# Kernel optimization log

Measured on AMD Instinct MI355X. Metric: run time of the kernel, lower is better.

The kernel has to match this reference:

```python
import jax, jax.numpy as jnp
import numpy as np

FACTOR = 5  # sampling factor from __init__


def setup_inputs() -> dict:
    key = jax.random.key(0)
    k1, k2, k3, k4 = jax.random.split(key, 4)
    B, L, H, D = 4, 2048, 8, 64
    S = min(FACTOR * int(np.ceil(np.log(L))), L)  # U_part = 40
    return {
        "queries": jax.random.normal(k1, (B, L, H, D), jnp.float32),
        "keys": jax.random.normal(k2, (B, L, H, D), jnp.float32),
        "values": jax.random.normal(k3, (B, L, H, D), jnp.float32),
        "index_sample": jax.random.randint(k4, (L, S), 0, L, jnp.int32),
    }


def reference(queries, keys, values, index_sample):
    B, L_Q, H, D = queries.shape
    L_K = keys.shape[1]
    Q = jnp.transpose(queries, (0, 2, 1, 3))  # [B,H,L_Q,D]
    K = jnp.transpose(keys, (0, 2, 1, 3))     # [B,H,L_K,D]
    V = jnp.transpose(values, (0, 2, 1, 3))   # [B,H,L_K,D]

    u = min(FACTOR * int(np.ceil(np.log(L_Q))), L_Q)  # n_top

    # --- _prob_QK: sampled QK to score queries, then top-u query selection ---
    # K_sample[b,h,q,s,:] = K[b,h,index_sample[q,s],:]  -> [B,H,L_Q,S,D]
    K_sample = K[:, :, index_sample, :]
    Q_K_sample = jnp.einsum('bhqd,bhqsd->bhqs', Q, K_sample)  # [B,H,L_Q,S]
    M = Q_K_sample.max(-1) - Q_K_sample.sum(-1) / L_K         # sparsity measure
    _, M_top = jax.lax.top_k(M, u)                            # [B,H,u] query indices

    Q_reduce = jnp.take_along_axis(Q, M_top[..., None], axis=2)  # [B,H,u,D]
    scale = 1.0 / np.sqrt(D)
    scores = jnp.einsum('bhud,bhkd->bhuk', Q_reduce, K) * scale  # [B,H,u,L_K]

    # --- _update_context causal mask: rows are the FIRST u rows of the full
    # triu(L_Q,L_Q) mask (faithful to original, which does NOT reindex by M_top)
    causal = jnp.triu(jnp.ones((u, L_Q), dtype=bool), 1)
    scores = jnp.where(causal[None, None], -jnp.inf, scores)
    attn = jax.nn.softmax(scores, axis=-1)
    upd = jnp.einsum('bhuk,bhkd->bhud', attn, V)  # [B,H,u,D]

    # --- _get_initial_context (mask_flag=True): running cumsum of V ---
    context = jnp.cumsum(V, axis=2)  # [B,H,L_Q,D]

    # scatter-overwrite selected query positions
    b = jnp.arange(B)[:, None, None]
    h = jnp.arange(H)[None, :, None]
    context = context.at[b, h, M_top].set(upd)

    return jnp.transpose(context, (0, 2, 1, 3))  # [B,L_Q,H,D]
```

## Files before the change

### kernel.cpp

```cpp
#include <hip/hip_runtime.h>
#include <stdint.h>

constexpr int B = 4;
constexpr int L = 2048;
constexpr int H = 8;
constexpr int D = 64;
constexpr int S = 40;
constexpr int U = 40;
constexpr int HD = H * D;
constexpr int NSEG = 8;
constexpr int SEGL = L / NSEG;
constexpr int NC = 64;
constexpr int CL = L / NC;

__device__ __forceinline__ unsigned mono(float v) {
    unsigned u = __float_as_uint(v);
    return (u & 0x80000000u) ? ~u : (u | 0x80000000u);
}

typedef float f4v __attribute__((ext_vector_type(4)));

__device__ __forceinline__ float4 ntload4(const float4* p) {
    f4v v = __builtin_nontemporal_load((const f4v*)p);
    return make_float4(v.x, v.y, v.z, v.w);
}

__global__ __launch_bounds__(256) void k_scores(
    const float4* __restrict__ Q4, const float4* __restrict__ K4,
    const int* __restrict__ idxs, float* __restrict__ M)
{
    int i = blockIdx.x;
    int xcd = i & 7;
    int b = xcd >> 1;
    int qc = (i >> 3) * 2 + (xcd & 1);
    int w = threadIdx.x >> 6;
    int lane = threadIdx.x & 63;
    int q = qc * 4 + w;
    int h = lane >> 3;
    int dd = lane & 7;

    const float4* qrow = Q4 + (size_t)(b * L + q) * 128;
    float4 qa = ntload4(qrow + 2 * lane);
    float4 qb = ntload4(qrow + 2 * lane + 1);

    int v_idx = idxs[q * S + (lane < S ? lane : 0)];

    const float4* kbase = K4 + (size_t)b * L * 128;
    float mx = -INFINITY, sm = 0.f;
    #pragma unroll 8
    for (int s = 0; s < S; ++s) {
        int ki = __shfl(v_idx, s);
        const float4* krow = kbase + (size_t)ki * 128;
        float4 ka = krow[2 * lane], kb = krow[2 * lane + 1];
        float d = qa.x * ka.x + qa.y * ka.y + qa.z * ka.z + qa.w * ka.w
                + qb.x * kb.x + qb.y * kb.y + qb.z * kb.z + qb.w * kb.w;
        d += __shfl_xor(d, 1);
        d += __shfl_xor(d, 2);
        d += __shfl_xor(d, 4);
        mx = fmaxf(mx, d);
        sm += d;
    }
    if (dd == 0)
        M[(b * 8 + h) * L + q] = mx - sm * (1.0f / (float)L);
}

__global__ __launch_bounds__(512) void k_topk_attn(
    const float* __restrict__ M, const float4* __restrict__ Q4,
    const float4* __restrict__ K4, const float4* __restrict__ V4,
    int* __restrict__ flags, float* __restrict__ upd)
{
    __shared__ unsigned long long cnd[NSEG * U];
    __shared__ int top_idx[U];
    __shared__ __align__(16) float Qs[U * 68];
    __shared__ __align__(16) float Ks[U * 68];
    __shared__ __align__(16) float Vs[U * 68];
    __shared__ float P[U * 41];

    int bh = blockIdx.x;
    int b = bh >> 3, h = bh & 7;
    int tid = threadIdx.x;
    int seg = tid >> 6, lane = tid & 63;

    int j0 = seg * SEGL + lane * 4;

    *(int4*)(flags + (size_t)bh * L + j0) = make_int4(0, 0, 0, 0);

    float4 v = *(const float4*)(M + (size_t)bh * L + j0);
    unsigned m[4] = { mono(v.x), mono(v.y), mono(v.z), mono(v.w) };
    int rank[4] = { 0, 0, 0, 0 };

    #pragma unroll 4
    for (int src = 0; src < 64; ++src) {
        #pragma unroll
        for (int slot = 0; slot < 4; ++slot) {
            unsigned bm = __shfl(m[slot], src);
            int bj = src * 4 + slot;
            #pragma unroll
            for (int s = 0; s < 4; ++s) {
                int myj = lane * 4 + s;
                rank[s] += (bm > m[s]) || (bm == m[s] && bj < myj);
            }
        }
    }
    #pragma unroll
    for (int s = 0; s < 4; ++s)
        if (rank[s] < U)
            cnd[seg * U + rank[s]] = ((unsigned long long)m[s] << 32)
                                   | (unsigned)(~(unsigned)(j0 + s));
    __syncthreads();

    {
        unsigned long long ka = cnd[tid < NSEG * U ? tid : 0];
        int ra = 0;
        for (int j = 0; j < NSEG * U; ++j) ra += (cnd[j] > ka);
        if (tid < NSEG * U && ra < U) top_idx[ra] = (int)(~(unsigned)ka);
    }
    __syncthreads();

    if (tid < U) flags[bh * L + top_idx[tid]] = tid + 1;

    for (int i = tid; i < U * 16; i += 512) {
        int r = i >> 4, d4 = i & 15;
        size_t kvbase = ((size_t)(b * L + r) * H + h) * 16 + d4;
        *(float4*)(Ks + r * 68 + d4 * 4) = K4[kvbase];
        *(float4*)(Vs + r * 68 + d4 * 4) = V4[kvbase];
        *(float4*)(Qs + r * 68 + d4 * 4) =
            Q4[((size_t)(b * L + top_idx[r]) * H + h) * 16 + d4];
    }
    __syncthreads();

    const float scale = 0.125f;
    for (int p = tid; p < U * U; p += 512) {
        int r = p / U, k = p - r * U;
        if (k <= r) {
            float acc = 0.f;
            #pragma unroll
            for (int d = 0; d < D; d += 4) {
                float4 a = *(const float4*)(Qs + r * 68 + d);
                float4 c = *(const float4*)(Ks + k * 68 + d);
                acc += a.x * c.x + a.y * c.y + a.z * c.z + a.w * c.w;
            }
            P[r * 41 + k] = acc * scale;
        }
    }
    __syncthreads();

    if (tid < U) {
        int r = tid;
        float mval = -INFINITY;
        for (int k = 0; k <= r; ++k) mval = fmaxf(mval, P[r * 41 + k]);
        float ssum = 0.f;
        for (int k = 0; k <= r; ++k) {
            float e = expf(P[r * 41 + k] - mval);
            P[r * 41 + k] = e;
            ssum += e;
        }
        float inv = 1.f / ssum;
        for (int k = 0; k <= r; ++k) P[r * 41 + k] *= inv;
    }
    __syncthreads();

    for (int t = tid; t < U * D; t += 512) {
        int r = t >> 6, d = t & 63;
        float acc = 0.f;
        for (int k = 0; k <= r; ++k) acc += P[r * 41 + k] * Vs[k * 68 + d];
        upd[((size_t)bh * U + r) * D + d] = acc;
    }
}

__global__ __launch_bounds__(512) void k_chunksum(
    const float* __restrict__ V, float* __restrict__ partial)
{
    int b = blockIdx.x >> 6;
    int c = blockIdx.x & 63;
    int hd = threadIdx.x;
    const float* vp = V + ((size_t)(b * L + c * CL)) * HD + hd;
    float s = 0.f;
    #pragma unroll
    for (int l = 0; l < CL; ++l) s += vp[(size_t)l * HD];
    partial[((size_t)b * NC + c) * HD + hd] = s;
}

__global__ __launch_bounds__(512) void k_out(
    const float* __restrict__ V, const float* __restrict__ partial,
    const int* __restrict__ flags, const float* __restrict__ upd,
    float* __restrict__ out)
{
    int b = blockIdx.x >> 6;
    int c = blockIdx.x & 63;
    int hd = threadIdx.x;
    int h = hd >> 6, d = hd & 63;

    float acc = 0.f;
    const float* pp = partial + (size_t)b * NC * HD + hd;
    for (int j = 0; j < c; ++j) acc += pp[(size_t)j * HD];

    const float* vp = V + ((size_t)(b * L + c * CL)) * HD + hd;
    float*       op = out + ((size_t)(b * L + c * CL)) * HD + hd;
    const int*   fp = flags + (b * H + h) * L + c * CL;
    const float* up = upd + (size_t)(b * H + h) * U * D + d;

    #pragma unroll 4
    for (int l = 0; l < CL; ++l) {
        acc += vp[(size_t)l * HD];
        int f = fp[l];
        float o = f ? up[(size_t)(f - 1) * D] : acc;
        __builtin_nontemporal_store(o, op + (size_t)l * HD);
    }
}

extern "C" void kernel_launch(void* const* d_in, const int* in_sizes, int n_in,
                              void* d_out, int out_size, void* d_ws, size_t ws_size,
                              hipStream_t stream)
{
    const float* Q   = (const float*)d_in[0];
    const float* K   = (const float*)d_in[1];
    const float* V   = (const float*)d_in[2];
    const int*  idxs = (const int*)d_in[3];
    float* out = (float*)d_out;

    char* ws = (char*)d_ws;
    float* M        = (float*)(ws);
    int*   flags    = (int*)  (ws + 262144);
    float* upd      = (float*)(ws + 524288);
    float* partial  = (float*)(ws + 851968);

    k_scores    <<<B * L / 4, 256, 0, stream>>>((const float4*)Q, (const float4*)K, idxs, M);
    k_topk_attn <<<B * H,     512, 0, stream>>>(M, (const float4*)Q, (const float4*)K,
                                                (const float4*)V, flags, upd);
    k_chunksum  <<<B * NC,    512, 0, stream>>>(V, partial);
    k_out       <<<B * NC,    512, 0, stream>>>(V, partial, flags, upd, out);
}
```

Baseline: 189.8 us.

## Fuse QK scores and softmax per wavefront with transposed K in LDS

Inside the top-k attention kernel, K is now stored transposed in shared memory, and each wavefront computes one full score row, one key per lane. The causal mask, max and sum reductions are done with cross-lane shuffles, which removes a separate barrier and a serial softmax loop that ran on only 40 threads. The PV product is unrolled with vectorized reads of the probability row. The cost is that every lane does the full 40-key work on padded, masked entries, and `__expf` slightly reduces exp accuracy.

```diff
diff --git a/kernel.cpp b/kernel.cpp
--- a/kernel.cpp
+++ b/kernel.cpp
@@ -72,15 +72,16 @@
     __shared__ unsigned long long cnd[NSEG * U];
     __shared__ int top_idx[U];
     __shared__ __align__(16) float Qs[U * 68];
-    __shared__ __align__(16) float Ks[U * 68];
+    __shared__ __align__(16) float Kst[64 * 65];
     __shared__ __align__(16) float Vs[U * 68];
-    __shared__ float P[U * 41];
+    __shared__ __align__(16) float Plds[U * 44];
 
     int bh = blockIdx.x;
     int b = bh >> 3, h = bh & 7;
     int tid = threadIdx.x;
-    int seg = tid >> 6, lane = tid & 63;
-
+    int wv = tid >> 6, lane = tid & 63;
+
+    int seg = wv;
     int j0 = seg * SEGL + lane * 4;
 
     *(int4*)(flags + (size_t)bh * L + j0) = make_int4(0, 0, 0, 0);
@@ -109,11 +110,12 @@
                                    | (unsigned)(~(unsigned)(j0 + s));
     __syncthreads();
 
-    {
-        unsigned long long ka = cnd[tid < NSEG * U ? tid : 0];
+    if (tid < NSEG * U) {
+        unsigned long long ka = cnd[tid];
         int ra = 0;
+        #pragma unroll 8
         for (int j = 0; j < NSEG * U; ++j) ra += (cnd[j] > ka);
-        if (tid < NSEG * U && ra < U) top_idx[ra] = (int)(~(unsigned)ka);
+        if (ra < U) top_idx[ra] = (int)(~(unsigned)ka);
     }
     __syncthreads();
 
@@ -122,7 +124,11 @@
     for (int i = tid; i < U * 16; i += 512) {
         int r = i >> 4, d4 = i & 15;
         size_t kvbase = ((size_t)(b * L + r) * H + h) * 16 + d4;
-        *(float4*)(Ks + r * 68 + d4 * 4) = K4[kvbase];
+        float4 kv = K4[kvbase];
+        Kst[(4 * d4 + 0) * 65 + r] = kv.x;
+        Kst[(4 * d4 + 1) * 65 + r] = kv.y;
+        Kst[(4 * d4 + 2) * 65 + r] = kv.z;
+        Kst[(4 * d4 + 3) * 65 + r] = kv.w;
         *(float4*)(Vs + r * 68 + d4 * 4) = V4[kvbase];
         *(float4*)(Qs + r * 68 + d4 * 4) =
             Q4[((size_t)(b * L + top_idx[r]) * H + h) * 16 + d4];
@@ -130,40 +136,44 @@
     __syncthreads();
 
     const float scale = 0.125f;
-    for (int p = tid; p < U * U; p += 512) {
-        int r = p / U, k = p - r * U;
-        if (k <= r) {
-            float acc = 0.f;
-            #pragma unroll
-            for (int d = 0; d < D; d += 4) {
-                float4 a = *(const float4*)(Qs + r * 68 + d);
-                float4 c = *(const float4*)(Ks + k * 68 + d);
-                acc += a.x * c.x + a.y * c.y + a.z * c.z + a.w * c.w;
-            }
-            P[r * 41 + k] = acc * scale;
+    int k = lane;
+    for (int rr = 0; rr < 5; ++rr) {
+        int r = wv * 5 + rr;
+        float acc = 0.f;
+        #pragma unroll
+        for (int d0 = 0; d0 < D; d0 += 4) {
+            float4 qv = *(const float4*)(Qs + r * 68 + d0);
+            acc += qv.x * Kst[(d0 + 0) * 65 + k];
+            acc += qv.y * Kst[(d0 + 1) * 65 + k];
+            acc += qv.z * Kst[(d0 + 2) * 65 + k];
+            acc += qv.w * Kst[(d0 + 3) * 65 + k];
         }
-    }
-    __syncthreads();
-
-    if (tid < U) {
-        int r = tid;
-        float mval = -INFINITY;
-        for (int k = 0; k <= r; ++k) mval = fmaxf(mval, P[r * 41 + k]);
-        float ssum = 0.f;
-        for (int k = 0; k <= r; ++k) {
-            float e = expf(P[r * 41 + k] - mval);
-            P[r * 41 + k] = e;
-            ssum += e;
-        }
-        float inv = 1.f / ssum;
-        for (int k = 0; k <= r; ++k) P[r * 41 + k] *= inv;
+        float sc = (k <= r) ? acc * scale : -INFINITY;
+        float mx = sc;
+        #pragma unroll
+        for (int off = 32; off >= 1; off >>= 1)
+            mx = fmaxf(mx, __shfl_xor(mx, off));
+        float e = __expf(sc - mx);
+        float sum = e;
+        #pragma unroll
+        for (int off = 32; off >= 1; off >>= 1)
+            sum += __shfl_xor(sum, off);
+        float p = e / sum;
+        if (k < U) Plds[r * 44 + k] = p;
     }
     __syncthreads();
 
     for (int t = tid; t < U * D; t += 512) {
         int r = t >> 6, d = t & 63;
         float acc = 0.f;
-        for (int k = 0; k <= r; ++k) acc += P[r * 41 + k] * Vs[k * 68 + d];
+        #pragma unroll
+        for (int kk = 0; kk < U; kk += 4) {
+            float4 pv = *(const float4*)(Plds + r * 44 + kk);
+            acc += pv.x * Vs[(kk + 0) * 68 + d];
+            acc += pv.y * Vs[(kk + 1) * 68 + d];
+            acc += pv.z * Vs[(kk + 2) * 68 + d];
+            acc += pv.w * Vs[(kk + 3) * 68 + d];
+        }
         upd[((size_t)bh * U + r) * D + d] = acc;
     }
 }
```

New measurement: 182.4 us. 1.04x faster.
